# Optimization experiments

Hardware: AMD Instinct MI355X
Metric: run time of the kernel (lower is better)

Reference implementation:

```python
import jax, jax.numpy as jnp
import numpy as np

T, B, D, H, Q = 512, 256, 128, 256, 8


def _qgate(z, params):
    # Exact closed form of the PennyLane circuit:
    #   RX(z_w); RX(params_w) per wire; CNOT chain + wraparound CNOT(n-1,0); <Z_0>
    # => <Z_0> = prod_{w=1..Q-1} cos(z_w + params_w)   (wire 0 cancels out)
    theta = z + params  # (B, Q)
    return jnp.prod(jnp.cos(theta[:, 1:]), axis=1, keepdims=True)  # (B, 1)


def setup_inputs() -> dict:
    key = jax.random.key(0)
    ks = jax.random.split(key, 16)
    inputs = jax.random.normal(ks[0], (T, B, D), dtype=jnp.float32)
    hx0 = jnp.zeros((B, H), dtype=jnp.float32)
    cx0 = jnp.zeros((B, H), dtype=jnp.float32)
    s = 1.0 / np.sqrt(D + H)
    def lin(k1, k2):
        W = jax.random.uniform(k1, (Q, D + H), jnp.float32, -s, s)
        b = jax.random.uniform(k2, (Q,), jnp.float32, -s, s)
        return W, b
    Wf, bf = lin(ks[1], ks[2]); pf = jax.random.normal(ks[3], (Q,), jnp.float32)
    Wi, bi = lin(ks[4], ks[5]); pi = jax.random.normal(ks[6], (Q,), jnp.float32)
    Wu, bu = lin(ks[7], ks[8]); pu = jax.random.normal(ks[9], (Q,), jnp.float32)
    Wo, bo = lin(ks[10], ks[11]); po = jax.random.normal(ks[12], (Q,), jnp.float32)
    return {"inputs": inputs, "hx0": hx0, "cx0": cx0,
            "Wf": Wf, "bf": bf, "pf": pf,
            "Wi": Wi, "bi": bi, "pi": pi,
            "Wu": Wu, "bu": bu, "pu": pu,
            "Wo": Wo, "bo": bo, "po": po}


def reference(inputs, hx0, cx0, Wf, bf, pf, Wi, bi, pi, Wu, bu, pu, Wo, bo, po):
    def step(carry, x):
        hx, cx = carry
        comb = jnp.concatenate([x, hx], axis=1)  # (B, D+H)
        f = jax.nn.sigmoid(_qgate(comb @ Wf.T + bf, pf))  # (B,1)
        i = jax.nn.sigmoid(_qgate(comb @ Wi.T + bi, pi))
        g = jnp.tanh(_qgate(comb @ Wu.T + bu, pu))
        o = jax.nn.sigmoid(_qgate(comb @ Wo.T + bo, po))
        cx = f * cx + i * g
        hx = o * jnp.tanh(cx)
        return (hx, cx), hx

    (hx, cx), outputs = jax.lax.scan(step, (hx0, cx0), inputs)
    return outputs, (hx, cx)
```

## Files before the change

kernel.cpp:

```cpp
#include <hip/hip_runtime.h>
#include <cstdint>

#define T 512
#define B 256
#define D 128
#define H 256
#define INV2PI 0.15915494309189535f

typedef float f32x4 __attribute__((ext_vector_type(4)));

#define WHS_OFF 0
#define HXS_OFF 64
#define CXF_OFF 131136
#define ZX_OFF  132096
#define ZX_FLOATS (T * B * 32)

__global__ __launch_bounds__(256) void k0_whs(const float* __restrict__ Wf, const float* __restrict__ Wi,
                                              const float* __restrict__ Wu, const float* __restrict__ Wo,
                                              float* __restrict__ whs) {
  int tid = threadIdx.x;
  int g = tid >> 6, r = tid & 63, q = r >> 3, part = r & 7;
  const float* W = (g == 0) ? Wf : (g == 1) ? Wi : (g == 2) ? Wu : Wo;
  const float* p = W + q * (D + H) + D + part * 32;
  float s = 0.f;
#pragma unroll
  for (int h = 0; h < 32; ++h) s += p[h];
  s += __shfl_xor(s, 1);
  s += __shfl_xor(s, 2);
  s += __shfl_xor(s, 4);
  if (part == 0) whs[g * 8 + q] = s * INV2PI;
}

__global__ __launch_bounds__(256) void k1_gemm(const float* __restrict__ x,
    const float* __restrict__ Wf, const float* __restrict__ bf, const float* __restrict__ pf,
    const float* __restrict__ Wi, const float* __restrict__ bi, const float* __restrict__ pi,
    const float* __restrict__ Wu, const float* __restrict__ bu, const float* __restrict__ pu,
    const float* __restrict__ Wo, const float* __restrict__ bo, const float* __restrict__ po,
    float* __restrict__ zx) {
  int tid = threadIdx.x;
  int tb = blockIdx.x * 256 + tid;
  const float4* xr = (const float4*)(x + (size_t)tb * D);

  const float* Ws[4] = {Wf, Wi, Wu, Wo};
  const float* bs[4] = {bf, bi, bu, bo};
  const float* ps[4] = {pf, pi, pu, po};

  float acc[4][7];
#pragma unroll
  for (int g = 0; g < 4; ++g)
#pragma unroll
    for (int j = 0; j < 7; ++j) acc[g][j] = 0.f;

#pragma unroll 2
  for (int k = 0; k < 32; ++k) {
    float4 xv = xr[k];
#pragma unroll
    for (int g = 0; g < 4; ++g) {
#pragma unroll
      for (int j = 0; j < 7; ++j) {
        const float4 wv = *(const float4*)(Ws[g] + (size_t)(j + 1) * (D + H) + k * 4);
        acc[g][j] = fmaf(xv.x, wv.x, fmaf(xv.y, wv.y, fmaf(xv.z, wv.z, fmaf(xv.w, wv.w, acc[g][j]))));
      }
    }
  }

  float4* zo = (float4*)(zx + (size_t)tb * 32);
#pragma unroll
  for (int g = 0; g < 4; ++g) {
    float z[7];
#pragma unroll
    for (int j = 0; j < 7; ++j)
      z[j] = fmaf(acc[g][j], INV2PI, (bs[g][j + 1] + ps[g][j + 1]) * INV2PI);
    zo[g * 2 + 0] = make_float4(0.f, z[0], z[1], z[2]);
    zo[g * 2 + 1] = make_float4(z[3], z[4], z[5], z[6]);
  }
}

__device__ __forceinline__ float qcos(float x) {
  return __builtin_amdgcn_cosf(__builtin_amdgcn_fractf(x));
}
#define QBCAST(v, CTRL) __int_as_float(__builtin_amdgcn_mov_dpp(__float_as_int(v), (CTRL), 0xF, 0xF, true))

#define STEP(S)                                                            \
  {                                                                        \
    float4 z0 = zA##S, z1 = zB##S;                                         \
    {                                                                      \
      size_t toff = (size_t)((t0 + S + 8) & (T - 1)) * 2048;               \
      zA##S = zp[toff];                                                    \
      zB##S = zp[toff + 1];                                                \
    }                                                                      \
    float c1 = qcos(fmaf(hx, w[0], z0.y));                                 \
    float c2 = qcos(fmaf(hx, w[1], z0.z));                                 \
    float c3 = qcos(fmaf(hx, w[2], z0.w));                                 \
    float c4 = qcos(fmaf(hx, w[3], z1.x));                                 \
    float c5 = qcos(fmaf(hx, w[4], z1.y));                                 \
    float c6 = qcos(fmaf(hx, w[5], z1.z));                                 \
    float c7 = qcos(fmaf(hx, w[6], z1.w));                                 \
    float pr = ((c1 * c2) * (c3 * c4)) * ((c5 * c6) * c7);                 \
    float e = __expf(pr * mk);                                             \
    float sv = __builtin_amdgcn_rcpf(1.f + e);                             \
    float val = fmaf(sv, sa, sb);                                          \
    float fv = QBCAST(val, 0x00);                                          \
    float iv = QBCAST(val, 0x55);                                          \
    float gv = QBCAST(val, 0xAA);                                          \
    float ov = QBCAST(val, 0xFF);                                          \
    cx = fmaf(fv, cx, iv * gv);                                            \
    float e2 = __expf(cx * -2.f);                                          \
    float tc = fmaf(__builtin_amdgcn_rcpf(1.f + e2), 2.f, -1.f);           \
    hx = ov * tc;                                                          \
    if (g == 0) hxs[(t0 + S) * B + b] = hx;                                \
  }

__global__ __launch_bounds__(64) void k2_scan(const float* __restrict__ zx, const float* __restrict__ whs,
                                              const float* __restrict__ hx0, const float* __restrict__ cx0,
                                              float* __restrict__ hxs, float* __restrict__ cxf) {
  int tid = threadIdx.x;
  int g = tid & 3;
  int b = blockIdx.x * 16 + (tid >> 2);

  float w[7];
#pragma unroll
  for (int j = 0; j < 7; ++j) w[j] = whs[g * 8 + 1 + j];
  bool isU = (g == 2);
  float mk = isU ? -2.f : -1.f;
  float sa = isU ? 2.f : 1.f;
  float sb = isU ? -1.f : 0.f;

  float hx = hx0[(size_t)b * H];
  float cx = cx0[(size_t)b * H];

  const float4* zp = (const float4*)zx + ((size_t)b * 8 + (size_t)g * 2);

  float4 zA0 = zp[0 * 2048], zB0 = zp[0 * 2048 + 1];
  float4 zA1 = zp[1 * 2048], zB1 = zp[1 * 2048 + 1];
  float4 zA2 = zp[2 * 2048], zB2 = zp[2 * 2048 + 1];
  float4 zA3 = zp[3 * 2048], zB3 = zp[3 * 2048 + 1];
  float4 zA4 = zp[4 * 2048], zB4 = zp[4 * 2048 + 1];
  float4 zA5 = zp[5 * 2048], zB5 = zp[5 * 2048 + 1];
  float4 zA6 = zp[6 * 2048], zB6 = zp[6 * 2048 + 1];
  float4 zA7 = zp[7 * 2048], zB7 = zp[7 * 2048 + 1];

  for (int t0 = 0; t0 < T; t0 += 8) {
    STEP(0)
    STEP(1)
    STEP(2)
    STEP(3)
    STEP(4)
    STEP(5)
    STEP(6)
    STEP(7)
  }
  if (g == 0) cxf[b] = cx;
}

__global__ __launch_bounds__(256) void k3_bcast(const float* __restrict__ hxs, const float* __restrict__ cxf,
                                                float* __restrict__ out) {
  const int TBH4 = (T * B * H) / 4;
  const int BH4 = (B * H) / 4;
  const int N4 = TBH4 + 2 * BH4;
  f32x4* out4 = (f32x4*)out;
  int stride = gridDim.x * blockDim.x;
  for (int i = blockIdx.x * blockDim.x + threadIdx.x; i < N4; i += stride) {
    float v;
    if (i < TBH4)            v = hxs[i >> 6];
    else if (i < TBH4 + BH4) v = hxs[(T - 1) * B + ((i - TBH4) >> 6)];
    else                     v = cxf[(i - TBH4 - BH4) >> 6];
    f32x4 pv = {v, v, v, v};
    __builtin_nontemporal_store(pv, &out4[i]);
  }
}

extern "C" void kernel_launch(void* const* d_in, const int* in_sizes, int n_in,
                              void* d_out, int out_size, void* d_ws, size_t ws_size,
                              hipStream_t stream) {
  const float* x   = (const float*)d_in[0];
  const float* hx0 = (const float*)d_in[1];
  const float* cx0 = (const float*)d_in[2];
  const float* Wf = (const float*)d_in[3];  const float* bf = (const float*)d_in[4];  const float* pf = (const float*)d_in[5];
  const float* Wi = (const float*)d_in[6];  const float* bi = (const float*)d_in[7];  const float* pi = (const float*)d_in[8];
  const float* Wu = (const float*)d_in[9];  const float* bu = (const float*)d_in[10]; const float* pu = (const float*)d_in[11];
  const float* Wo = (const float*)d_in[12]; const float* bo = (const float*)d_in[13]; const float* po = (const float*)d_in[14];

  float* wsf = (float*)d_ws;
  float* whs = wsf + WHS_OFF;
  float* hxs = wsf + HXS_OFF;
  float* cxf = wsf + CXF_OFF;
  float* out = (float*)d_out;
  float* zx = (ws_size >= (size_t)(ZX_OFF + ZX_FLOATS) * sizeof(float))
                  ? (wsf + ZX_OFF)
                  : (out + ((size_t)out_size - ZX_FLOATS));

  hipLaunchKernelGGL(k0_whs, dim3(1), dim3(256), 0, stream, Wf, Wi, Wu, Wo, whs);
  hipLaunchKernelGGL(k1_gemm, dim3(512), dim3(256), 0, stream,
                     x, Wf, bf, pf, Wi, bi, pi, Wu, bu, pu, Wo, bo, po, zx);
  hipLaunchKernelGGL(k2_scan, dim3(16), dim3(64), 0, stream, zx, whs, hx0, cx0, hxs, cxf);
  hipLaunchKernelGGL(k3_bcast, dim3(4096), dim3(256), 0, stream, hxs, cxf, out);
}
```

Measured before the change: 358.3 us.

## Stage scan inputs through LDS with async double-buffering and retile projection GEMM

The scan kernel now pulls 16-timestep tiles of precomputed gate pre-activations into shared memory using global_load_lds, double-buffered with explicit vmcnt waits. Each timestep then reads its inputs from LDS instead of from strided global loads, and the hidden-state stores are batched at the end of each tile. The projection GEMM caches pre-scaled weights in LDS and has each thread handle four rows to reuse those weights, and the exponentials are folded into exp2f. The intent is to take global memory latency off the serial recurrence critical path. The cost is manual waitcnt bookkeeping and extra register pressure in the GEMM.

```diff
diff --git a/kernel.cpp b/kernel.cpp
--- a/kernel.cpp
+++ b/kernel.cpp
@@ -5,7 +5,9 @@
 #define B 256
 #define D 128
 #define H 256
+#define DH 384
 #define INV2PI 0.15915494309189535f
+#define NLOG2E 1.442695041f
 
 typedef float f32x4 __attribute__((ext_vector_type(4)));
 
@@ -21,7 +23,7 @@
   int tid = threadIdx.x;
   int g = tid >> 6, r = tid & 63, q = r >> 3, part = r & 7;
   const float* W = (g == 0) ? Wf : (g == 1) ? Wi : (g == 2) ? Wu : Wo;
-  const float* p = W + q * (D + H) + D + part * 32;
+  const float* p = W + q * DH + D + part * 32;
   float s = 0.f;
 #pragma unroll
   for (int h = 0; h < 32; ++h) s += p[h];
@@ -31,49 +33,68 @@
   if (part == 0) whs[g * 8 + q] = s * INV2PI;
 }
 
-__global__ __launch_bounds__(256) void k1_gemm(const float* __restrict__ x,
+__global__ __launch_bounds__(128) void k1_gemm(const float* __restrict__ x,
     const float* __restrict__ Wf, const float* __restrict__ bf, const float* __restrict__ pf,
     const float* __restrict__ Wi, const float* __restrict__ bi, const float* __restrict__ pi,
     const float* __restrict__ Wu, const float* __restrict__ bu, const float* __restrict__ pu,
     const float* __restrict__ Wo, const float* __restrict__ bo, const float* __restrict__ po,
     float* __restrict__ zx) {
+  __shared__ float wl[28 * 128];
+  __shared__ float offs[32];
   int tid = threadIdx.x;
-  int tb = blockIdx.x * 256 + tid;
-  const float4* xr = (const float4*)(x + (size_t)tb * D);
-
   const float* Ws[4] = {Wf, Wi, Wu, Wo};
   const float* bs[4] = {bf, bi, bu, bo};
   const float* ps[4] = {pf, pi, pu, po};
-
-  float acc[4][7];
 #pragma unroll
   for (int g = 0; g < 4; ++g)
-#pragma unroll
-    for (int j = 0; j < 7; ++j) acc[g][j] = 0.f;
-
-#pragma unroll 2
+    for (int i = tid; i < 896; i += 128) {
+      int q = i >> 7, d = i & 127;
+      wl[g * 896 + i] = Ws[g][(q + 1) * DH + d] * INV2PI;
+    }
+  if (tid < 32) {
+    int g = tid >> 3, q = tid & 7;
+    offs[tid] = (bs[g][q] + ps[g][q]) * INV2PI;
+  }
+  __syncthreads();
+
+  int row0 = blockIdx.x * 512 + tid;
+  const float4* x4 = (const float4*)x;
+  const float4* wl4 = (const float4*)wl;
+
+  float acc0[28], acc1[28], acc2[28], acc3[28];
+#pragma unroll
+  for (int r = 0; r < 28; ++r) acc0[r] = acc1[r] = acc2[r] = acc3[r] = 0.f;
+
   for (int k = 0; k < 32; ++k) {
-    float4 xv = xr[k];
-#pragma unroll
-    for (int g = 0; g < 4; ++g) {
-#pragma unroll
-      for (int j = 0; j < 7; ++j) {
-        const float4 wv = *(const float4*)(Ws[g] + (size_t)(j + 1) * (D + H) + k * 4);
-        acc[g][j] = fmaf(xv.x, wv.x, fmaf(xv.y, wv.y, fmaf(xv.z, wv.z, fmaf(xv.w, wv.w, acc[g][j]))));
-      }
-    }
-  }
-
-  float4* zo = (float4*)(zx + (size_t)tb * 32);
-#pragma unroll
-  for (int g = 0; g < 4; ++g) {
-    float z[7];
-#pragma unroll
-    for (int j = 0; j < 7; ++j)
-      z[j] = fmaf(acc[g][j], INV2PI, (bs[g][j + 1] + ps[g][j + 1]) * INV2PI);
-    zo[g * 2 + 0] = make_float4(0.f, z[0], z[1], z[2]);
-    zo[g * 2 + 1] = make_float4(z[3], z[4], z[5], z[6]);
-  }
+    float4 xv0 = x4[(size_t)row0 * 32 + k];
+    float4 xv1 = x4[(size_t)row0 * 32 + 4096 + k];
+    float4 xv2 = x4[(size_t)row0 * 32 + 8192 + k];
+    float4 xv3 = x4[(size_t)row0 * 32 + 12288 + k];
+#pragma unroll
+    for (int r = 0; r < 28; ++r) {
+      float4 wv = wl4[r * 32 + k];
+      acc0[r] = fmaf(xv0.x, wv.x, fmaf(xv0.y, wv.y, fmaf(xv0.z, wv.z, fmaf(xv0.w, wv.w, acc0[r]))));
+      acc1[r] = fmaf(xv1.x, wv.x, fmaf(xv1.y, wv.y, fmaf(xv1.z, wv.z, fmaf(xv1.w, wv.w, acc1[r]))));
+      acc2[r] = fmaf(xv2.x, wv.x, fmaf(xv2.y, wv.y, fmaf(xv2.z, wv.z, fmaf(xv2.w, wv.w, acc2[r]))));
+      acc3[r] = fmaf(xv3.x, wv.x, fmaf(xv3.y, wv.y, fmaf(xv3.z, wv.z, fmaf(xv3.w, wv.w, acc3[r]))));
+    }
+  }
+
+#define WROW(ACC, M)                                                                     \
+  {                                                                                      \
+    float4* zo = (float4*)(zx + (size_t)(row0 + (M)*128) * 32);                          \
+    _Pragma("unroll") for (int g = 0; g < 4; ++g) {                                      \
+      zo[g * 2 + 0] = make_float4(0.f, ACC[g * 7 + 0] + offs[g * 8 + 1],                 \
+                                  ACC[g * 7 + 1] + offs[g * 8 + 2],                      \
+                                  ACC[g * 7 + 2] + offs[g * 8 + 3]);                     \
+      zo[g * 2 + 1] = make_float4(ACC[g * 7 + 3] + offs[g * 8 + 4],                      \
+                                  ACC[g * 7 + 4] + offs[g * 8 + 5],                      \
+                                  ACC[g * 7 + 5] + offs[g * 8 + 6],                      \
+                                  ACC[g * 7 + 6] + offs[g * 8 + 7]);                     \
+    }                                                                                    \
+  }
+  WROW(acc0, 0) WROW(acc1, 1) WROW(acc2, 2) WROW(acc3, 3)
+#undef WROW
 }
 
 __device__ __forceinline__ float qcos(float x) {
@@ -81,23 +102,39 @@
 }
 #define QBCAST(v, CTRL) __int_as_float(__builtin_amdgcn_mov_dpp(__float_as_int(v), (CTRL), 0xF, 0xF, true))
 
-#define STEP(S)                                                            \
+__device__ __forceinline__ void gload16(const float* g, float* l, int tid) {
+#if __has_builtin(__builtin_amdgcn_global_load_lds)
+  __builtin_amdgcn_global_load_lds((const __attribute__((address_space(1))) unsigned int*)g,
+                                   (__attribute__((address_space(3))) unsigned int*)l, 16, 0, 0);
+#else
+  *(f32x4*)(l + tid * 4) = *(const f32x4*)g;
+#endif
+}
+
+__device__ __forceinline__ void stage_tile(const float* gbase, int t0, float* lbase, int tid) {
+#pragma unroll
+  for (int s = 0; s < 16; ++s) {
+    const float* g = gbase + (size_t)(t0 + s) * 8192;
+    gload16(g, lbase + s * 512, tid);
+    gload16(g + 256, lbase + s * 512 + 256, tid);
+  }
+}
+
+#define STEP(S, ZA, ZB, TGT, TOFF)                                         \
   {                                                                        \
-    float4 z0 = zA##S, z1 = zB##S;                                         \
-    {                                                                      \
-      size_t toff = (size_t)((t0 + S + 8) & (T - 1)) * 2048;               \
-      zA##S = zp[toff];                                                    \
-      zB##S = zp[toff + 1];                                                \
-    }                                                                      \
-    float c1 = qcos(fmaf(hx, w[0], z0.y));                                 \
-    float c2 = qcos(fmaf(hx, w[1], z0.z));                                 \
-    float c3 = qcos(fmaf(hx, w[2], z0.w));                                 \
-    float c4 = qcos(fmaf(hx, w[3], z1.x));                                 \
-    float c5 = qcos(fmaf(hx, w[4], z1.y));                                 \
-    float c6 = qcos(fmaf(hx, w[5], z1.z));                                 \
-    float c7 = qcos(fmaf(hx, w[6], z1.w));                                 \
-    float pr = ((c1 * c2) * (c3 * c4)) * ((c5 * c6) * c7);                 \
-    float e = __expf(pr * mk);                                             \
+    f32x4 z0 = ZA, z1 = ZB;                                                \
+    ZA = *(const f32x4*)((TGT) + (TOFF));                                  \
+    ZB = *(const f32x4*)((TGT) + (TOFF) + 4);                              \
+    float c1 = qcos(fmaf(hx, w[0], z0[1]));                                \
+    float c2 = qcos(fmaf(hx, w[1], z0[2]));                                \
+    float c3 = qcos(fmaf(hx, w[2], z0[3]));                                \
+    float c4 = qcos(fmaf(hx, w[3], z1[0]));                                \
+    float c5 = qcos(fmaf(hx, w[4], z1[1]));                                \
+    float c6 = qcos(fmaf(hx, w[5], z1[2]));                                \
+    float c7 = qcos(fmaf(hx, w[6], z1[3]));                                \
+    float d4 = c7 * mk2;                                                   \
+    float pr = ((c1 * c2) * (c3 * c4)) * ((c5 * c6) * d4);                 \
+    float e = exp2f(pr);                                                   \
     float sv = __builtin_amdgcn_rcpf(1.f + e);                             \
     float val = fmaf(sv, sa, sb);                                          \
     float fv = QBCAST(val, 0x00);                                          \
@@ -105,50 +142,81 @@
     float gv = QBCAST(val, 0xAA);                                          \
     float ov = QBCAST(val, 0xFF);                                          \
     cx = fmaf(fv, cx, iv * gv);                                            \
-    float e2 = __expf(cx * -2.f);                                          \
+    float e2 = exp2f(cx * -2.885390082f);                                  \
     float tc = fmaf(__builtin_amdgcn_rcpf(1.f + e2), 2.f, -1.f);           \
     hx = ov * tc;                                                          \
-    if (g == 0) hxs[(t0 + S) * B + b] = hx;                                \
+    h##S = hx;                                                             \
   }
 
 __global__ __launch_bounds__(64) void k2_scan(const float* __restrict__ zx, const float* __restrict__ whs,
                                               const float* __restrict__ hx0, const float* __restrict__ cx0,
                                               float* __restrict__ hxs, float* __restrict__ cxf) {
+  __shared__ float zbuf[2 * 16 * 16 * 32];
   int tid = threadIdx.x;
   int g = tid & 3;
-  int b = blockIdx.x * 16 + (tid >> 2);
+  int c = tid >> 2;
+  int b = blockIdx.x * 16 + c;
 
   float w[7];
 #pragma unroll
   for (int j = 0; j < 7; ++j) w[j] = whs[g * 8 + 1 + j];
   bool isU = (g == 2);
-  float mk = isU ? -2.f : -1.f;
+  float mk2 = isU ? -2.885390082f : -NLOG2E;
   float sa = isU ? 2.f : 1.f;
   float sb = isU ? -1.f : 0.f;
 
   float hx = hx0[(size_t)b * H];
   float cx = cx0[(size_t)b * H];
 
-  const float4* zp = (const float4*)zx + ((size_t)b * 8 + (size_t)g * 2);
-
-  float4 zA0 = zp[0 * 2048], zB0 = zp[0 * 2048 + 1];
-  float4 zA1 = zp[1 * 2048], zB1 = zp[1 * 2048 + 1];
-  float4 zA2 = zp[2 * 2048], zB2 = zp[2 * 2048 + 1];
-  float4 zA3 = zp[3 * 2048], zB3 = zp[3 * 2048 + 1];
-  float4 zA4 = zp[4 * 2048], zB4 = zp[4 * 2048 + 1];
-  float4 zA5 = zp[5 * 2048], zB5 = zp[5 * 2048 + 1];
-  float4 zA6 = zp[6 * 2048], zB6 = zp[6 * 2048 + 1];
-  float4 zA7 = zp[7 * 2048], zB7 = zp[7 * 2048 + 1];
-
-  for (int t0 = 0; t0 < T; t0 += 8) {
-    STEP(0)
-    STEP(1)
-    STEP(2)
-    STEP(3)
-    STEP(4)
-    STEP(5)
-    STEP(6)
-    STEP(7)
+  float* zb = &zbuf[0];
+  float* lb = zb + tid * 8;
+  const float* gbase = zx + (size_t)blockIdx.x * 512 + (size_t)tid * 4;
+
+  stage_tile(gbase, 0, zb, tid);
+  stage_tile(gbase, 16, zb + 8192, tid);
+  asm volatile("s_waitcnt vmcnt(32)" ::: "memory");
+
+  f32x4 pA = *(const f32x4*)(lb + 0);
+  f32x4 pB = *(const f32x4*)(lb + 4);
+  f32x4 qA = *(const f32x4*)(lb + 512);
+  f32x4 qB = *(const f32x4*)(lb + 516);
+
+  float h0, h1, h2, h3, h4, h5, h6, h7, h8, h9, h10, h11, h12, h13, h14, h15;
+
+  for (int kt = 0; kt < 32; ++kt) {
+    float* bp = lb + (kt & 1) * 8192;
+    float* bq = lb + ((kt & 1) ^ 1) * 8192;
+
+    STEP(0, pA, pB, bp, 2 * 512)
+    STEP(1, qA, qB, bp, 3 * 512)
+    STEP(2, pA, pB, bp, 4 * 512)
+    STEP(3, qA, qB, bp, 5 * 512)
+    STEP(4, pA, pB, bp, 6 * 512)
+    STEP(5, qA, qB, bp, 7 * 512)
+    STEP(6, pA, pB, bp, 8 * 512)
+    STEP(7, qA, qB, bp, 9 * 512)
+    STEP(8, pA, pB, bp, 10 * 512)
+    STEP(9, qA, qB, bp, 11 * 512)
+    STEP(10, pA, pB, bp, 12 * 512)
+    STEP(11, qA, qB, bp, 13 * 512)
+    STEP(12, pA, pB, bp, 14 * 512)
+    STEP(13, qA, qB, bp, 15 * 512)
+    asm volatile("s_waitcnt vmcnt(0)" ::: "memory");
+    STEP(14, pA, pB, bq, 0 * 512)
+    STEP(15, qA, qB, bq, 1 * 512)
+
+    if (g == 0) {
+      float* hp = hxs + (size_t)(kt * 16) * B + b;
+      hp[0 * B] = h0;   hp[1 * B] = h1;   hp[2 * B] = h2;   hp[3 * B] = h3;
+      hp[4 * B] = h4;   hp[5 * B] = h5;   hp[6 * B] = h6;   hp[7 * B] = h7;
+      hp[8 * B] = h8;   hp[9 * B] = h9;   hp[10 * B] = h10; hp[11 * B] = h11;
+      hp[12 * B] = h12; hp[13 * B] = h13; hp[14 * B] = h14; hp[15 * B] = h15;
+    }
+
+    if (kt + 2 < 32) {
+      asm volatile("s_waitcnt lgkmcnt(0)" ::: "memory");
+      stage_tile(gbase, (kt + 2) * 16, zb + (kt & 1) * 8192, tid);
+    }
   }
   if (g == 0) cxf[b] = cx;
 }
@@ -191,7 +259,7 @@
                   : (out + ((size_t)out_size - ZX_FLOATS));
 
   hipLaunchKernelGGL(k0_whs, dim3(1), dim3(256), 0, stream, Wf, Wi, Wu, Wo, whs);
-  hipLaunchKernelGGL(k1_gemm, dim3(512), dim3(256), 0, stream,
+  hipLaunchKernelGGL(k1_gemm, dim3(256), dim3(128), 0, stream,
                      x, Wf, bf, pf, Wi, bi, pi, Wu, bu, pu, Wo, bo, po, zx);
   hipLaunchKernelGGL(k2_scan, dim3(16), dim3(64), 0, stream, zx, whs, hx0, cx0, hxs, cxf);
   hipLaunchKernelGGL(k3_bcast, dim3(4096), dim3(256), 0, stream, hxs, cxf, out);
```

After: 348.0 us. 1.03x faster.
